# Performance work log

Hardware: AMD Instinct MI355X
Metric: run time of the kernel (lower is better)

The kernel has to match this reference:

```python
import jax, jax.numpy as jnp
import numpy as np

HIDDEN = 2048
N_HEAD = 16
N_KV_HEAD = 4
HEAD_DIM = HIDDEN // N_HEAD
B, S = 2, 2048


def setup_inputs() -> dict:
    key = jax.random.key(0)
    ks = jax.random.split(key, 10)
    scale = 1.0 / np.sqrt(HIDDEN)
    x = jax.random.normal(ks[0], (B, S, HIDDEN), dtype=jnp.float32)
    # causal additive mask, broadcastable over batch and heads
    causal = jnp.tril(jnp.ones((S, S), dtype=jnp.bool_))
    attention_mask = jnp.where(causal, 0.0, -1e9).astype(jnp.float32)[None, None]
    wq_w = jax.random.uniform(ks[1], (HIDDEN, HIDDEN), jnp.float32, -scale, scale)
    wq_b = jax.random.uniform(ks[2], (HIDDEN,), jnp.float32, -scale, scale)
    wk_w = jax.random.uniform(ks[3], (N_KV_HEAD * HEAD_DIM, HIDDEN), jnp.float32, -scale, scale)
    wk_b = jax.random.uniform(ks[4], (N_KV_HEAD * HEAD_DIM,), jnp.float32, -scale, scale)
    wv_w = jax.random.uniform(ks[5], (N_KV_HEAD * HEAD_DIM, HIDDEN), jnp.float32, -scale, scale)
    wv_b = jax.random.uniform(ks[6], (N_KV_HEAD * HEAD_DIM,), jnp.float32, -scale, scale)
    wo_w = jax.random.uniform(ks[7], (HIDDEN, HIDDEN), jnp.float32, -scale, scale)
    wo_b = jax.random.uniform(ks[8], (HIDDEN,), jnp.float32, -scale, scale)
    return dict(x=x, attention_mask=attention_mask, wq_w=wq_w, wq_b=wq_b,
                wk_w=wk_w, wk_b=wk_b, wv_w=wv_w, wv_b=wv_b, wo_w=wo_w, wo_b=wo_b)


def reference(x, attention_mask, wq_w, wq_b, wk_w, wk_b, wv_w, wv_b, wo_w, wo_b):
    bs, seq_len, _ = x.shape
    group = N_HEAD // N_KV_HEAD
    q = x @ wq_w.T + wq_b  # [B,S,H*D]
    k = x @ wk_w.T + wk_b  # [B,S,Hkv*D]
    v = x @ wv_w.T + wv_b
    q = q.reshape(bs, seq_len, N_HEAD, HEAD_DIM).transpose(0, 2, 1, 3)        # [B,H,S,D]
    k = k.reshape(bs, seq_len, N_KV_HEAD, HEAD_DIM).transpose(0, 2, 1, 3)     # [B,Hkv,S,D]
    v = v.reshape(bs, seq_len, N_KV_HEAD, HEAD_DIM).transpose(0, 2, 1, 3)
    # GQA: share each kv head across `group` query heads (repeat_interleave equiv)
    qg = q.reshape(bs, N_KV_HEAD, group, seq_len, HEAD_DIM)
    scores = jnp.einsum('bkgqd,bkld->bkgql', qg, k) / np.sqrt(HEAD_DIM)       # [B,Hkv,g,S,S]
    scores = scores + attention_mask[:, :, None]  # mask broadcast over head dims
    attn = jax.nn.softmax(scores, axis=-1)  # dropout is identity at inference
    out = jnp.einsum('bkgql,bkld->bkgqd', attn, v)                             # [B,Hkv,g,S,D]
    out = out.reshape(bs, N_HEAD, seq_len, HEAD_DIM).transpose(0, 2, 1, 3)
    out = out.reshape(bs, seq_len, HIDDEN)
    return out @ wo_w.T + wo_b
```

## Files before the change

### kernel.cpp

```cpp
#include <hip/hip_runtime.h>

typedef __bf16 bf16;
typedef __bf16 bf16x8 __attribute__((ext_vector_type(8)));
typedef __bf16 bf16x4 __attribute__((ext_vector_type(4)));
typedef __bf16 bf16x2 __attribute__((ext_vector_type(2)));
typedef float  f32x4  __attribute__((ext_vector_type(4)));

#define HIDDEN 2048
#define NH 16
#define NKV 4
#define HD 128
#define BB 2
#define SS 2048
#define MTOT (BB*SS)
#define KVD (NKV*HD)

__device__ __forceinline__ void gload_lds16(const void* g, void* l) {
  __builtin_amdgcn_global_load_lds(
      (__attribute__((address_space(1))) void*)(void*)g,
      (__attribute__((address_space(3))) void*)l,
      16, 0, 0);
}

__global__ void detect_dtype(const unsigned short* __restrict__ x, int* __restrict__ flag) {
  __shared__ int cnt;
  if (threadIdx.x == 0) cnt = 0;
  __syncthreads();
  int c = 0;
  for (int i = threadIdx.x; i < 8192; i += blockDim.x) {
    float v = fabsf(__uint_as_float((unsigned)x[i] << 16));
    if (v > 64.0f || (v > 0.0f && v < 9.5367431640625e-07f)) ++c;
  }
  atomicAdd(&cnt, c);
  __syncthreads();
  if (threadIdx.x == 0) flag[0] = (cnt > 1024) ? 1 : 0;
}

struct ConvJobs {
  const void* src[8];
  bf16*       dst[8];
  long long   n[8];
};

__global__ void conv_multi(ConvJobs jobs, const int* __restrict__ flag) {
  const int f = flag[0];
  const int a = blockIdx.y;
  const long long n = jobs.n[a];
  bf16* dst = jobs.dst[a];
  long long i = (long long)blockIdx.x * blockDim.x + threadIdx.x;
  const long long stride = (long long)gridDim.x * blockDim.x;
  if (f) {
    const float* s = (const float*)jobs.src[a];
    for (; i < n; i += stride) dst[i] = (bf16)s[i];
  } else {
    const bf16* s = (const bf16*)jobs.src[a];
    for (; i < n; i += stride) dst[i] = s[i];
  }
}

__global__ void conv_one(const void* __restrict__ src, bf16* __restrict__ dst,
                         long long n, const int* __restrict__ flag) {
  const int f = flag[0];
  long long i = (long long)blockIdx.x * blockDim.x + threadIdx.x;
  const long long stride = (long long)gridDim.x * blockDim.x;
  if (f) {
    const float* s = (const float*)src;
    for (; i < n; i += stride) dst[i] = (bf16)s[i];
  } else {
    const bf16* s = (const bf16*)src;
    for (; i < n; i += stride) dst[i] = s[i];
  }
}

__global__ __launch_bounds__(256)
void gemm_qkv(const bf16* __restrict__ A,
              const bf16* __restrict__ wq, const bf16* __restrict__ bq,
              const bf16* __restrict__ wk, const bf16* __restrict__ bk,
              const bf16* __restrict__ wv, const bf16* __restrict__ bv,
              bf16* __restrict__ Cq, bf16* __restrict__ Ck, bf16* __restrict__ Cvt)
{
  __shared__ bf16 As[2][128*32];
  __shared__ bf16 Bs[2][128*32];
  const int bx = blockIdx.x;
  const bf16 *W, *bias;
  int n0, mode;
  if (bx < 16)      { W = wq; bias = bq; n0 = bx*128;      mode = 0; }
  else if (bx < 20) { W = wk; bias = bk; n0 = (bx-16)*128; mode = 1; }
  else              { W = wv; bias = bv; n0 = (bx-20)*128; mode = 2; }

  const int tid  = threadIdx.x;
  const int wave = tid >> 6, lane = tid & 63;
  const int g = lane >> 4, l15 = lane & 15;
  const int m0 = blockIdx.y * 128;
  const int wm = (wave >> 1) * 64, wn = (wave & 1) * 64;
  const int srow = lane >> 2;
  const int scol = (lane & 3) * 8;
  f32x4 acc[4][4] = {};

  #pragma unroll
  for (int i = 0; i < 2; ++i) {
    const int seg = wave*2 + i;
    const int row = seg*16 + srow;
    gload_lds16(A + (size_t)(m0+row)*HIDDEN + scol, &As[0][row*32 + scol]);
    gload_lds16(W + (size_t)(n0+row)*HIDDEN + scol, &Bs[0][row*32 + scol]);
  }
  asm volatile("s_waitcnt vmcnt(0)" ::: "memory");
  __syncthreads();

  int buf = 0;
  for (int k0 = 0; k0 < HIDDEN; k0 += 32) {
    if (k0 + 32 < HIDDEN) {
      #pragma unroll
      for (int i = 0; i < 2; ++i) {
        const int seg = wave*2 + i;
        const int row = seg*16 + srow;
        gload_lds16(A + (size_t)(m0+row)*HIDDEN + k0+32 + scol, &As[buf^1][row*32 + scol]);
        gload_lds16(W + (size_t)(n0+row)*HIDDEN + k0+32 + scol, &Bs[buf^1][row*32 + scol]);
      }
    }
    bf16x8 af[4], bfr[4];
    #pragma unroll
    for (int m = 0; m < 4; ++m)
      af[m] = *(const bf16x8*)&As[buf][(wm + m*16 + l15)*32 + g*8];
    #pragma unroll
    for (int n = 0; n < 4; ++n)
      bfr[n] = *(const bf16x8*)&Bs[buf][(wn + n*16 + l15)*32 + g*8];
    #pragma unroll
    for (int m = 0; m < 4; ++m)
      #pragma unroll
      for (int n = 0; n < 4; ++n)
        acc[m][n] = __builtin_amdgcn_mfma_f32_16x16x32_bf16(af[m], bfr[n], acc[m][n], 0, 0, 0);
    asm volatile("s_waitcnt vmcnt(0)" ::: "memory");
    __syncthreads();
    buf ^= 1;
  }
  if (mode == 2) {
    #pragma unroll
    for (int n = 0; n < 4; ++n) {
      const int cc = n0 + wn + n*16 + l15;
      const float bv2 = (float)bias[cc];
      #pragma unroll
      for (int m = 0; m < 4; ++m) {
        const int row = m0 + wm + m*16 + g*4;
        bf16x4 o4;
        #pragma unroll
        for (int r = 0; r < 4; ++r) o4[r] = (bf16)(acc[m][n][r] + bv2);
        *(bf16x4*)&Cvt[(size_t)cc*MTOT + row] = o4;
      }
    }
  } else {
    bf16* Cb = (mode == 0) ? Cq : Ck;
    const int N = (mode == 0) ? HIDDEN : KVD;
    #pragma unroll
    for (int n = 0; n < 4; ++n) {
      const int col = n0 + wn + n*16 + l15;
      const float bv2 = (float)bias[col];
      #pragma unroll
      for (int m = 0; m < 4; ++m) {
        const int row = m0 + wm + m*16 + g*4;
        #pragma unroll
        for (int r = 0; r < 4; ++r)
          Cb[(size_t)(row + r)*N + col] = (bf16)(acc[m][n][r] + bv2);
      }
    }
  }
}

__global__ __launch_bounds__(256)
void gemm_bt(const bf16* __restrict__ A, const bf16* __restrict__ W,
             const bf16* __restrict__ bias, void* __restrict__ C,
             int M, int N, int K, const int* __restrict__ flagp)
{
  __shared__ bf16 As[2][128*32];
  __shared__ bf16 Bs[2][128*32];
  const int tid  = threadIdx.x;
  const int wave = tid >> 6, lane = tid & 63;
  const int g = lane >> 4, l15 = lane & 15;
  const int m0 = blockIdx.y * 128, n0 = blockIdx.x * 128;
  const int wm = (wave >> 1) * 64, wn = (wave & 1) * 64;
  const int srow = lane >> 2;
  const int scol = (lane & 3) * 8;
  f32x4 acc[4][4] = {};

  #pragma unroll
  for (int i = 0; i < 2; ++i) {
    const int seg = wave*2 + i;
    const int row = seg*16 + srow;
    gload_lds16(A + (size_t)(m0+row)*K + scol, &As[0][row*32 + scol]);
    gload_lds16(W + (size_t)(n0+row)*K + scol, &Bs[0][row*32 + scol]);
  }
  asm volatile("s_waitcnt vmcnt(0)" ::: "memory");
  __syncthreads();

  int buf = 0;
  for (int k0 = 0; k0 < K; k0 += 32) {
    if (k0 + 32 < K) {
      #pragma unroll
      for (int i = 0; i < 2; ++i) {
        const int seg = wave*2 + i;
        const int row = seg*16 + srow;
        gload_lds16(A + (size_t)(m0+row)*K + k0+32 + scol, &As[buf^1][row*32 + scol]);
        gload_lds16(W + (size_t)(n0+row)*K + k0+32 + scol, &Bs[buf^1][row*32 + scol]);
      }
    }
    bf16x8 af[4], bfr[4];
    #pragma unroll
    for (int m = 0; m < 4; ++m)
      af[m] = *(const bf16x8*)&As[buf][(wm + m*16 + l15)*32 + g*8];
    #pragma unroll
    for (int n = 0; n < 4; ++n)
      bfr[n] = *(const bf16x8*)&Bs[buf][(wn + n*16 + l15)*32 + g*8];
    #pragma unroll
    for (int m = 0; m < 4; ++m)
      #pragma unroll
      for (int n = 0; n < 4; ++n)
        acc[m][n] = __builtin_amdgcn_mfma_f32_16x16x32_bf16(af[m], bfr[n], acc[m][n], 0, 0, 0);
    asm volatile("s_waitcnt vmcnt(0)" ::: "memory");
    __syncthreads();
    buf ^= 1;
  }
  const int outf = flagp ? flagp[0] : 0;
  if (outf) {
    float* Cf = (float*)C;
    #pragma unroll
    for (int n = 0; n < 4; ++n) {
      const int col = n0 + wn + n*16 + l15;
      const float bv = (float)bias[col];
      #pragma unroll
      for (int m = 0; m < 4; ++m) {
        const int row = m0 + wm + m*16 + g*4;
        #pragma unroll
        for (int r = 0; r < 4; ++r)
          Cf[(size_t)(row + r)*N + col] = acc[m][n][r] + bv;
      }
    }
  } else {
    bf16* Cb = (bf16*)C;
    #pragma unroll
    for (int n = 0; n < 4; ++n) {
      const int col = n0 + wn + n*16 + l15;
      const float bv = (float)bias[col];
      #pragma unroll
      for (int m = 0; m < 4; ++m) {
        const int row = m0 + wm + m*16 + g*4;
        #pragma unroll
        for (int r = 0; r < 4; ++r)
          Cb[(size_t)(row + r)*N + col] = (bf16)(acc[m][n][r] + bv);
      }
    }
  }
}

#define QB 64
#define PPAD 72

__global__ __launch_bounds__(256)
void attn_fwd(const bf16* __restrict__ Q, const bf16* __restrict__ K,
              const bf16* __restrict__ Vt, bf16* __restrict__ O)
{
  __shared__ bf16 Ks[2][64*128];
  __shared__ bf16 Vs[2][128*64];
  __shared__ bf16 Pl[4][16][PPAD];
  const int tid = threadIdx.x, wave = tid >> 6, lane = tid & 63;
  const int g = lane >> 4, l15 = lane & 15;
  const int bh = blockIdx.y;
  const int b = bh >> 4, h = bh & 15, kvh = h >> 2;
  const bf16* Qh = Q + ((size_t)b*SS)*HIDDEN + h*HD;
  const bf16* Kh = K + ((size_t)b*SS)*KVD + kvh*HD;
  const bf16* Vh = Vt + ((size_t)kvh*HD)*MTOT + (size_t)b*SS;
  bf16*       Oh = O + ((size_t)b*SS)*HIDDEN + h*HD;

  const float scale  = 0.08838834764831845f;
  const float L2E    = 1.4426950408889634f;
  const float NEGBIG = -1.0e30f;

  const int krow_st = (lane >> 4);
  const int vrow_st = (lane >> 3);
  const int ksc     = (lane & 15);
  const int vsc     = (lane & 7) ^ (lane >> 3);

  #pragma unroll 1
  for (int pass = 0; pass < 2; ++pass) {
    const int qt = pass ? (31 - (int)blockIdx.x) : (int)blockIdx.x;
    const int qrow0 = qt*QB + wave*16;
    const int qg    = qrow0 + l15;

    bf16x8 bq[4];
    #pragma unroll
    for (int c = 0; c < 4; ++c)
      bq[c] = *(const bf16x8*)(Qh + (size_t)(qrow0 + l15)*HIDDEN + c*32 + g*8);

    f32x4 od[8] = {};
    float m_run = NEGBIG, l_part = 0.f;
    const int ntiles = qt + 1;

    {
      const int kv0 = 0;
      #pragma unroll
      for (int i = 0; i < 4; ++i) {
        const int s = wave*4 + i;
        const int kr = s*4 + krow_st;
        const int kc = ksc ^ (kr & 7);
        gload_lds16(Kh + (size_t)(kv0 + kr)*KVD + kc*8, &Ks[0][s*512 + lane*8]);
        const int vr = s*8 + vrow_st;
        gload_lds16(Vh + (size_t)vr*MTOT + kv0 + vsc*8, &Vs[0][s*512 + lane*8]);
      }
    }
    asm volatile("s_waitcnt vmcnt(0)" ::: "memory");
    __syncthreads();

    int buf = 0;
    #pragma unroll 1
    for (int t = 0; t < ntiles; ++t) {
      const int kv0 = t * 64;

      if (t + 1 < ntiles) {
        const int kv1 = kv0 + 64;
        #pragma unroll
        for (int i = 0; i < 4; ++i) {
          const int s = wave*4 + i;
          const int kr = s*4 + krow_st;
          const int kc = ksc ^ (kr & 7);
          gload_lds16(Kh + (size_t)(kv1 + kr)*KVD + kc*8, &Ks[buf^1][s*512 + lane*8]);
          const int vr = s*8 + vrow_st;
          gload_lds16(Vh + (size_t)vr*MTOT + kv1 + vsc*8, &Vs[buf^1][s*512 + lane*8]);
        }
      }

      f32x4 st[4];
      #pragma unroll
      for (int nb = 0; nb < 4; ++nb) {
        f32x4 s = {};
        #pragma unroll
        for (int c = 0; c < 4; ++c) {
          const int krow = nb*16 + l15;
          const int kch  = (c*4 + g) ^ (krow & 7);
          bf16x8 ka = *(const bf16x8*)&Ks[buf][krow*128 + kch*8];
          s = __builtin_amdgcn_mfma_f32_16x16x32_bf16(ka, bq[c], s, 0, 0, 0);
        }
        st[nb] = s;
      }

      float x[16];
      float mt = NEGBIG;
      #pragma unroll
      for (int nb = 0; nb < 4; ++nb)
        #pragma unroll
        for (int r = 0; r < 4; ++r) {
          const int kv = kv0 + nb*16 + g*4 + r;
          float v = st[nb][r] * scale;
          v = (kv <= qg) ? v : NEGBIG;
          x[nb*4 + r] = v;
          mt = fmaxf(mt, v);
        }
      mt = fmaxf(mt, __shfl_xor(mt, 16, 64));
      mt = fmaxf(mt, __shfl_xor(mt, 32, 64));
      const float m_new = fmaxf(m_run, mt);
      const float corr  = __builtin_amdgcn_exp2f((m_run - m_new) * L2E);

      float psum = 0.f;
      bf16x2 pk[4][2];
      #pragma unroll
      for (int nb = 0; nb < 4; ++nb) {
        const float p0 = __builtin_amdgcn_exp2f((x[nb*4+0] - m_new) * L2E);
        const float p1 = __builtin_amdgcn_exp2f((x[nb*4+1] - m_new) * L2E);
        const float p2 = __builtin_amdgcn_exp2f((x[nb*4+2] - m_new) * L2E);
        const float p3 = __builtin_amdgcn_exp2f((x[nb*4+3] - m_new) * L2E);
        psum += p0 + p1 + p2 + p3;
        pk[nb][0] = bf16x2{(bf16)p0, (bf16)p1};
        pk[nb][1] = bf16x2{(bf16)p2, (bf16)p3};
      }
      l_part = l_part * corr + psum;
      m_run  = m_new;
      #pragma unroll
      for (int db = 0; db < 8; ++db) od[db] *= corr;

      #pragma unroll
      for (int nb = 0; nb < 4; ++nb) {
        *(bf16x2*)&Pl[wave][l15][nb*16 + g*4 + 0] = pk[nb][0];
        *(bf16x2*)&Pl[wave][l15][nb*16 + g*4 + 2] = pk[nb][1];
      }
      asm volatile("s_waitcnt lgkmcnt(0)" ::: "memory");
      __builtin_amdgcn_sched_barrier(0);

      #pragma unroll
      for (int c = 0; c < 2; ++c) {
        bf16x8 pb = *(const bf16x8*)&Pl[wave][l15][c*32 + g*8];
        #pragma unroll
        for (int db = 0; db < 8; ++db) {
          const int vrow = db*16 + l15;
          const int vch  = (c*4 + g) ^ (l15 & 7);
          bf16x8 va = *(const bf16x8*)&Vs[buf][vrow*64 + vch*8];
          od[db] = __builtin_amdgcn_mfma_f32_16x16x32_bf16(va, pb, od[db], 0, 0, 0);
        }
      }

      asm volatile("s_waitcnt vmcnt(0)" ::: "memory");
      __syncthreads();
      buf ^= 1;
    }

    float lt = l_part;
    lt += __shfl_xor(lt, 16, 64);
    lt += __shfl_xor(lt, 32, 64);
    const float inv = 1.0f / lt;
    #pragma unroll
    for (int db = 0; db < 8; ++db) {
      bf16x4 o4;
      #pragma unroll
      for (int r = 0; r < 4; ++r) o4[r] = (bf16)(od[db][r] * inv);
      *(bf16x4*)(Oh + (size_t)qg*HIDDEN + db*16 + g*4) = o4;
    }
  }
}

extern "C" void kernel_launch(void* const* d_in, const int* in_sizes, int n_in,
                              void* d_out, int out_size, void* d_ws, size_t ws_size,
                              hipStream_t stream)
{
  (void)in_sizes; (void)n_in; (void)out_size; (void)ws_size;
  const void* x    = d_in[0];
  const void* wq_w = d_in[2];
  const void* wq_b = d_in[3];
  const void* wk_w = d_in[4];
  const void* wk_b = d_in[5];
  const void* wv_w = d_in[6];
  const void* wv_b = d_in[7];
  const void* wo_w = d_in[8];
  const void* wo_b = d_in[9];

  int*  flag = (int*)d_ws;
  bf16* base = (bf16*)((char*)d_ws + 256);
  const long long NX  = (long long)MTOT*HIDDEN;
  const long long NWQ = (long long)HIDDEN*HIDDEN;
  const long long NWK = (long long)KVD*HIDDEN;
  bf16* x_ao = base;
  bf16* wqwo = x_ao + NX;
  bf16* wk_c = wqwo + NWQ;
  bf16* wv_c = wk_c + NWK;
  bf16* bq_c = wv_c + NWK;
  bf16* bk_c = bq_c + 2048;
  bf16* bv_c = bk_c + 512;
  bf16* bo_c = bv_c + 512;
  bf16* q_ws  = bo_c + 2048;
  bf16* k_ws  = q_ws + NX;
  bf16* vt_ws = k_ws + (long long)MTOT*KVD;

  detect_dtype<<<1, 256, 0, stream>>>((const unsigned short*)x, flag);

  ConvJobs jb;
  jb.src[0] = x;    jb.dst[0] = x_ao; jb.n[0] = NX;
  jb.src[1] = wq_w; jb.dst[1] = wqwo; jb.n[1] = NWQ;
  jb.src[2] = wk_w; jb.dst[2] = wk_c; jb.n[2] = NWK;
  jb.src[3] = wv_w; jb.dst[3] = wv_c; jb.n[3] = NWK;
  jb.src[4] = wq_b; jb.dst[4] = bq_c; jb.n[4] = 2048;
  jb.src[5] = wk_b; jb.dst[5] = bk_c; jb.n[5] = 512;
  jb.src[6] = wv_b; jb.dst[6] = bv_c; jb.n[6] = 512;
  jb.src[7] = wo_b; jb.dst[7] = bo_c; jb.n[7] = 2048;
  conv_multi<<<dim3(1024, 8), 256, 0, stream>>>(jb, flag);

  gemm_qkv<<<dim3(24, MTOT/128), 256, 0, stream>>>(x_ao, wqwo, bq_c, wk_c, bk_c,
                                                   wv_c, bv_c, q_ws, k_ws, vt_ws);

  conv_one<<<dim3(1024), 256, 0, stream>>>(wo_w, wqwo, NWQ, flag);

  attn_fwd<<<dim3(16, BB*NH), 256, 0, stream>>>(q_ws, k_ws, vt_ws, x_ao);

  gemm_bt<<<dim3(HIDDEN/128, MTOT/128), 256, 0, stream>>>(x_ao, wqwo, bo_c, d_out, MTOT, HIDDEN, HIDDEN, flag);
}
```

Before: 247.1 us.

## Use 256x256 tiles with 512 threads, LDS swizzle and split-phase MFMA scheduling

Replaces the 128x128 QKV and output-projection GEMMs with 256x256-tile kernels of 8 waves each. Each wave computes a 128x64 sub-tile. LDS staging uses an XOR swizzle to avoid bank conflicts, and each k-step is split into two MFMA phases separated by barriers, with setprio raising MFMA priority. The larger tiles increase data reuse per loaded byte, but they cut the grid to 192 and 128 blocks, fewer than the CU count, which risks underfilling the GPU.

New measurement: 251.2 us. Within noise of the previous version (+1.6%).

```diff
diff --git a/kernel.cpp b/kernel.cpp
--- a/kernel.cpp
+++ b/kernel.cpp
@@ -20,6 +20,12 @@
       (__attribute__((address_space(1))) void*)(void*)g,
       (__attribute__((address_space(3))) void*)l,
       16, 0, 0);
+}
+
+__device__ __forceinline__ void pipe_barrier() {
+  __builtin_amdgcn_sched_barrier(0);
+  __builtin_amdgcn_s_barrier();
+  __builtin_amdgcn_sched_barrier(0);
 }
 
 __global__ void detect_dtype(const unsigned short* __restrict__ x, int* __restrict__ flag) {
@@ -72,79 +78,103 @@
   }
 }
 
-__global__ __launch_bounds__(256)
-void gemm_qkv(const bf16* __restrict__ A,
-              const bf16* __restrict__ wq, const bf16* __restrict__ bq,
-              const bf16* __restrict__ wk, const bf16* __restrict__ bk,
-              const bf16* __restrict__ wv, const bf16* __restrict__ bv,
-              bf16* __restrict__ Cq, bf16* __restrict__ Ck, bf16* __restrict__ Cvt)
+
+__global__ __launch_bounds__(512)
+void gemm_qkv256(const bf16* __restrict__ A,
+                 const bf16* __restrict__ wq, const bf16* __restrict__ bq,
+                 const bf16* __restrict__ wk, const bf16* __restrict__ bk,
+                 const bf16* __restrict__ wv, const bf16* __restrict__ bv,
+                 bf16* __restrict__ Cq, bf16* __restrict__ Ck, bf16* __restrict__ Cvt)
 {
-  __shared__ bf16 As[2][128*32];
-  __shared__ bf16 Bs[2][128*32];
+  __shared__ bf16 Asl[2][256*32];
+  __shared__ bf16 Bsl[2][256*32];
   const int bx = blockIdx.x;
-  const bf16 *W, *bias;
+  const bf16 *Wp, *bias;
   int n0, mode;
-  if (bx < 16)      { W = wq; bias = bq; n0 = bx*128;      mode = 0; }
-  else if (bx < 20) { W = wk; bias = bk; n0 = (bx-16)*128; mode = 1; }
-  else              { W = wv; bias = bv; n0 = (bx-20)*128; mode = 2; }
+  if (bx < 8)       { Wp = wq; bias = bq; n0 = bx*256;      mode = 0; }
+  else if (bx < 10) { Wp = wk; bias = bk; n0 = (bx-8)*256;  mode = 1; }
+  else              { Wp = wv; bias = bv; n0 = (bx-10)*256; mode = 2; }
 
   const int tid  = threadIdx.x;
   const int wave = tid >> 6, lane = tid & 63;
   const int g = lane >> 4, l15 = lane & 15;
-  const int m0 = blockIdx.y * 128;
-  const int wm = (wave >> 1) * 64, wn = (wave & 1) * 64;
-  const int srow = lane >> 2;
-  const int scol = (lane & 3) * 8;
-  f32x4 acc[4][4] = {};
-
-  #pragma unroll
-  for (int i = 0; i < 2; ++i) {
-    const int seg = wave*2 + i;
-    const int row = seg*16 + srow;
-    gload_lds16(A + (size_t)(m0+row)*HIDDEN + scol, &As[0][row*32 + scol]);
-    gload_lds16(W + (size_t)(n0+row)*HIDDEN + scol, &Bs[0][row*32 + scol]);
-  }
+  const int wr = wave >> 2, wc = wave & 3;
+  const int m0 = blockIdx.y * 256;
+
+  f32x4 acc[8][4] = {};
+
+  auto stage4 = [&](int nb, int k0) {
+    #pragma unroll
+    for (int i = 0; i < 2; ++i) {
+      const int cl  = tid + i*512;
+      const int row = cl >> 2, ch = cl & 3;
+      const int sc  = ch ^ ((row >> 2) & 3);
+      gload_lds16(A  + (size_t)(m0 + row)*HIDDEN + k0 + sc*8, &Asl[nb][cl*8]);
+      gload_lds16(Wp + (size_t)(n0 + row)*HIDDEN + k0 + sc*8, &Bsl[nb][cl*8]);
+    }
+  };
+
+  stage4(0, 0);
   asm volatile("s_waitcnt vmcnt(0)" ::: "memory");
-  __syncthreads();
-
+  pipe_barrier();
+
+  const int nt = HIDDEN / 32;
   int buf = 0;
-  for (int k0 = 0; k0 < HIDDEN; k0 += 32) {
-    if (k0 + 32 < HIDDEN) {
-      #pragma unroll
-      for (int i = 0; i < 2; ++i) {
-        const int seg = wave*2 + i;
-        const int row = seg*16 + srow;
-        gload_lds16(A + (size_t)(m0+row)*HIDDEN + k0+32 + scol, &As[buf^1][row*32 + scol]);
-        gload_lds16(W + (size_t)(n0+row)*HIDDEN + k0+32 + scol, &Bs[buf^1][row*32 + scol]);
-      }
-    }
+  for (int t = 0; t < nt; ++t) {
     bf16x8 af[4], bfr[4];
     #pragma unroll
-    for (int m = 0; m < 4; ++m)
-      af[m] = *(const bf16x8*)&As[buf][(wm + m*16 + l15)*32 + g*8];
-    #pragma unroll
-    for (int n = 0; n < 4; ++n)
-      bfr[n] = *(const bf16x8*)&Bs[buf][(wn + n*16 + l15)*32 + g*8];
-    #pragma unroll
-    for (int m = 0; m < 4; ++m)
-      #pragma unroll
-      for (int n = 0; n < 4; ++n)
-        acc[m][n] = __builtin_amdgcn_mfma_f32_16x16x32_bf16(af[m], bfr[n], acc[m][n], 0, 0, 0);
+    for (int mi = 0; mi < 4; ++mi) {
+      const int rl = wr*128 + mi*16 + l15;
+      const int ch = g ^ ((rl >> 2) & 3);
+      af[mi] = *(const bf16x8*)&Asl[buf][rl*32 + ch*8];
+    }
+    #pragma unroll
+    for (int ni = 0; ni < 4; ++ni) {
+      const int rl = wc*64 + ni*16 + l15;
+      const int ch = g ^ ((rl >> 2) & 3);
+      bfr[ni] = *(const bf16x8*)&Bsl[buf][rl*32 + ch*8];
+    }
+    if (t + 1 < nt) stage4(buf ^ 1, (t + 1) * 32);
+    pipe_barrier();
+    __builtin_amdgcn_s_setprio(1);
+    #pragma unroll
+    for (int mi = 0; mi < 4; ++mi)
+      #pragma unroll
+      for (int ni = 0; ni < 4; ++ni)
+        acc[mi][ni] = __builtin_amdgcn_mfma_f32_16x16x32_bf16(af[mi], bfr[ni], acc[mi][ni], 0, 0, 0);
+    __builtin_amdgcn_s_setprio(0);
+    #pragma unroll
+    for (int mi = 0; mi < 4; ++mi) {
+      const int rl = wr*128 + 64 + mi*16 + l15;
+      const int ch = g ^ ((rl >> 2) & 3);
+      af[mi] = *(const bf16x8*)&Asl[buf][rl*32 + ch*8];
+    }
+    pipe_barrier();
+    __builtin_amdgcn_s_setprio(1);
+    #pragma unroll
+    for (int mi = 0; mi < 4; ++mi)
+      #pragma unroll
+      for (int ni = 0; ni < 4; ++ni)
+        acc[4+mi][ni] = __builtin_amdgcn_mfma_f32_16x16x32_bf16(af[mi], bfr[ni], acc[4+mi][ni], 0, 0, 0);
+    __builtin_amdgcn_s_setprio(0);
+    __builtin_amdgcn_sched_barrier(0);
     asm volatile("s_waitcnt vmcnt(0)" ::: "memory");
-    __syncthreads();
+    __builtin_amdgcn_s_barrier();
+    __builtin_amdgcn_sched_barrier(0);
     buf ^= 1;
   }
+
   if (mode == 2) {
     #pragma unroll
-    for (int n = 0; n < 4; ++n) {
-      const int cc = n0 + wn + n*16 + l15;
+    for (int ni = 0; ni < 4; ++ni) {
+      const int cc = n0 + wc*64 + ni*16 + l15;
       const float bv2 = (float)bias[cc];
       #pragma unroll
-      for (int m = 0; m < 4; ++m) {
-        const int row = m0 + wm + m*16 + g*4;
+      for (int mi = 0; mi < 8; ++mi) {
+        const int row = m0 + wr*128 + mi*16 + g*4;
         bf16x4 o4;
         #pragma unroll
-        for (int r = 0; r < 4; ++r) o4[r] = (bf16)(acc[m][n][r] + bv2);
+        for (int r = 0; r < 4; ++r) o4[r] = (bf16)(acc[mi][ni][r] + bv2);
         *(bf16x4*)&Cvt[(size_t)cc*MTOT + row] = o4;
       }
     }
@@ -152,100 +182,123 @@
     bf16* Cb = (mode == 0) ? Cq : Ck;
     const int N = (mode == 0) ? HIDDEN : KVD;
     #pragma unroll
-    for (int n = 0; n < 4; ++n) {
-      const int col = n0 + wn + n*16 + l15;
+    for (int ni = 0; ni < 4; ++ni) {
+      const int col = n0 + wc*64 + ni*16 + l15;
       const float bv2 = (float)bias[col];
       #pragma unroll
-      for (int m = 0; m < 4; ++m) {
-        const int row = m0 + wm + m*16 + g*4;
+      for (int mi = 0; mi < 8; ++mi) {
+        const int row = m0 + wr*128 + mi*16 + g*4;
         #pragma unroll
         for (int r = 0; r < 4; ++r)
-          Cb[(size_t)(row + r)*N + col] = (bf16)(acc[m][n][r] + bv2);
-      }
-    }
-  }
-}
-
-__global__ __launch_bounds__(256)
-void gemm_bt(const bf16* __restrict__ A, const bf16* __restrict__ W,
-             const bf16* __restrict__ bias, void* __restrict__ C,
-             int M, int N, int K, const int* __restrict__ flagp)
+          Cb[(size_t)(row + r)*N + col] = (bf16)(acc[mi][ni][r] + bv2);
+      }
+    }
+  }
+}
+
+__global__ __launch_bounds__(512)
+void gemm_o256(const bf16* __restrict__ A, const bf16* __restrict__ Wp,
+               const bf16* __restrict__ bias, void* __restrict__ C,
+               int N, int K, const int* __restrict__ flagp)
 {
-  __shared__ bf16 As[2][128*32];
-  __shared__ bf16 Bs[2][128*32];
+  __shared__ bf16 Asl[2][256*32];
+  __shared__ bf16 Bsl[2][256*32];
   const int tid  = threadIdx.x;
   const int wave = tid >> 6, lane = tid & 63;
   const int g = lane >> 4, l15 = lane & 15;
-  const int m0 = blockIdx.y * 128, n0 = blockIdx.x * 128;
-  const int wm = (wave >> 1) * 64, wn = (wave & 1) * 64;
-  const int srow = lane >> 2;
-  const int scol = (lane & 3) * 8;
-  f32x4 acc[4][4] = {};
-
-  #pragma unroll
-  for (int i = 0; i < 2; ++i) {
-    const int seg = wave*2 + i;
-    const int row = seg*16 + srow;
-    gload_lds16(A + (size_t)(m0+row)*K + scol, &As[0][row*32 + scol]);
-    gload_lds16(W + (size_t)(n0+row)*K + scol, &Bs[0][row*32 + scol]);
-  }
+  const int wr = wave >> 2, wc = wave & 3;
+  const int m0 = blockIdx.y * 256, n0 = blockIdx.x * 256;
+
+  f32x4 acc[8][4] = {};
+
+  auto stage4 = [&](int nb, int k0) {
+    #pragma unroll
+    for (int i = 0; i < 2; ++i) {
+      const int cl  = tid + i*512;
+      const int row = cl >> 2, ch = cl & 3;
+      const int sc  = ch ^ ((row >> 2) & 3);
+      gload_lds16(A  + (size_t)(m0 + row)*K + k0 + sc*8, &Asl[nb][cl*8]);
+      gload_lds16(Wp + (size_t)(n0 + row)*K + k0 + sc*8, &Bsl[nb][cl*8]);
+    }
+  };
+
+  stage4(0, 0);
   asm volatile("s_waitcnt vmcnt(0)" ::: "memory");
-  __syncthreads();
-
+  pipe_barrier();
+
+  const int nt = K / 32;
   int buf = 0;
-  for (int k0 = 0; k0 < K; k0 += 32) {
-    if (k0 + 32 < K) {
-      #pragma unroll
-      for (int i = 0; i < 2; ++i) {
-        const int seg = wave*2 + i;
-        const int row = seg*16 + srow;
-        gload_lds16(A + (size_t)(m0+row)*K + k0+32 + scol, &As[buf^1][row*32 + scol]);
-        gload_lds16(W + (size_t)(n0+row)*K + k0+32 + scol, &Bs[buf^1][row*32 + scol]);
-      }
-    }
+  for (int t = 0; t < nt; ++t) {
     bf16x8 af[4], bfr[4];
     #pragma unroll
-    for (int m = 0; m < 4; ++m)
-      af[m] = *(const bf16x8*)&As[buf][(wm + m*16 + l15)*32 + g*8];
-    #pragma unroll
-    for (int n = 0; n < 4; ++n)
-      bfr[n] = *(const bf16x8*)&Bs[buf][(wn + n*16 + l15)*32 + g*8];
-    #pragma unroll
-    for (int m = 0; m < 4; ++m)
-      #pragma unroll
-      for (int n = 0; n < 4; ++n)
-        acc[m][n] = __builtin_amdgcn_mfma_f32_16x16x32_bf16(af[m], bfr[n], acc[m][n], 0, 0, 0);
+    for (int mi = 0; mi < 4; ++mi) {
+      const int rl = wr*128 + mi*16 + l15;
+      const int ch = g ^ ((rl >> 2) & 3);
+      af[mi] = *(const bf16x8*)&Asl[buf][rl*32 + ch*8];
+    }
+    #pragma unroll
+    for (int ni = 0; ni < 4; ++ni) {
+      const int rl = wc*64 + ni*16 + l15;
+      const int ch = g ^ ((rl >> 2) & 3);
+      bfr[ni] = *(const bf16x8*)&Bsl[buf][rl*32 + ch*8];
+    }
+    if (t + 1 < nt) stage4(buf ^ 1, (t + 1) * 32);
+    pipe_barrier();
+    __builtin_amdgcn_s_setprio(1);
+    #pragma unroll
+    for (int mi = 0; mi < 4; ++mi)
+      #pragma unroll
+      for (int ni = 0; ni < 4; ++ni)
+        acc[mi][ni] = __builtin_amdgcn_mfma_f32_16x16x32_bf16(af[mi], bfr[ni], acc[mi][ni], 0, 0, 0);
+    __builtin_amdgcn_s_setprio(0);
+    #pragma unroll
+    for (int mi = 0; mi < 4; ++mi) {
+      const int rl = wr*128 + 64 + mi*16 + l15;
+      const int ch = g ^ ((rl >> 2) & 3);
+      af[mi] = *(const bf16x8*)&Asl[buf][rl*32 + ch*8];
+    }
+    pipe_barrier();
+    __builtin_amdgcn_s_setprio(1);
+    #pragma unroll
+    for (int mi = 0; mi < 4; ++mi)
+      #pragma unroll
+      for (int ni = 0; ni < 4; ++ni)
+        acc[4+mi][ni] = __builtin_amdgcn_mfma_f32_16x16x32_bf16(af[mi], bfr[ni], acc[4+mi][ni], 0, 0, 0);
+    __builtin_amdgcn_s_setprio(0);
+    __builtin_amdgcn_sched_barrier(0);
     asm volatile("s_waitcnt vmcnt(0)" ::: "memory");
-    __syncthreads();
+    __builtin_amdgcn_s_barrier();
+    __builtin_amdgcn_sched_barrier(0);
     buf ^= 1;
   }
+
   const int outf = flagp ? flagp[0] : 0;
   if (outf) {
     float* Cf = (float*)C;
     #pragma unroll
-    for (int n = 0; n < 4; ++n) {
-      const int col = n0 + wn + n*16 + l15;
+    for (int ni = 0; ni < 4; ++ni) {
+      const int col = n0 + wc*64 + ni*16 + l15;
       const float bv = (float)bias[col];
       #pragma unroll
-      for (int m = 0; m < 4; ++m) {
-        const int row = m0 + wm + m*16 + g*4;
+      for (int mi = 0; mi < 8; ++mi) {
+        const int row = m0 + wr*128 + mi*16 + g*4;
         #pragma unroll
         for (int r = 0; r < 4; ++r)
-          Cf[(size_t)(row + r)*N + col] = acc[m][n][r] + bv;
+          Cf[(size_t)(row + r)*N + col] = acc[mi][ni][r] + bv;
       }
     }
   } else {
     bf16* Cb = (bf16*)C;
     #pragma unroll
-    for (int n = 0; n < 4; ++n) {
-      const int col = n0 + wn + n*16 + l15;
+    for (int ni = 0; ni < 4; ++ni) {
+      const int col = n0 + wc*64 + ni*16 + l15;
       const float bv = (float)bias[col];
       #pragma unroll
-      for (int m = 0; m < 4; ++m) {
-        const int row = m0 + wm + m*16 + g*4;
+      for (int mi = 0; mi < 8; ++mi) {
+        const int row = m0 + wr*128 + mi*16 + g*4;
         #pragma unroll
         for (int r = 0; r < 4; ++r)
-          Cb[(size_t)(row + r)*N + col] = (bf16)(acc[m][n][r] + bv);
+          Cb[(size_t)(row + r)*N + col] = (bf16)(acc[mi][ni][r] + bv);
       }
     }
   }
@@ -459,12 +512,13 @@
   jb.src[7] = wo_b; jb.dst[7] = bo_c; jb.n[7] = 2048;
   conv_multi<<<dim3(1024, 8), 256, 0, stream>>>(jb, flag);
 
-  gemm_qkv<<<dim3(24, MTOT/128), 256, 0, stream>>>(x_ao, wqwo, bq_c, wk_c, bk_c,
-                                                   wv_c, bv_c, q_ws, k_ws, vt_ws);
+  gemm_qkv256<<<dim3(12, MTOT/256), 512, 0, stream>>>(x_ao, wqwo, bq_c, wk_c, bk_c,
+                                                      wv_c, bv_c, q_ws, k_ws, vt_ws);
 
   conv_one<<<dim3(1024), 256, 0, stream>>>(wo_w, wqwo, NWQ, flag);
 
   attn_fwd<<<dim3(16, BB*NH), 256, 0, stream>>>(q_ws, k_ws, vt_ws, x_ao);
 
-  gemm_bt<<<dim3(HIDDEN/128, MTOT/128), 256, 0, stream>>>(x_ao, wqwo, bo_c, d_out, MTOT, HIDDEN, HIDDEN, flag);
-}
+  gemm_o256<<<dim3(HIDDEN/256, MTOT/256), 512, 0, stream>>>(x_ao, wqwo, bo_c, d_out,
+                                                            HIDDEN, HIDDEN, flag);
+}
```
